# Kernel tuning notes

Hardware: AMD Instinct MI355X
Metric: run time of the kernel (lower is better)

## Reference

```python
import jax, jax.numpy as jnp
import numpy as np

N_NODES = 100000
N_EDGES = 1600000
N_GRAPHS = 1000
H = 4

def _ln(x, g, b, eps=1e-5):
    m = x.mean(-1, keepdims=True)
    v = ((x - m) ** 2).mean(-1, keepdims=True)
    return (x - m) / jnp.sqrt(v + eps) * g + b

def _gat(x, src, dst, W, att_src, att_dst, bias, C):
    # PyG GATConv (self-loops already appended to src/dst): per-edge scores,
    # segment softmax over incoming edges of each dst node, scatter-add aggregation.
    N = x.shape[0]
    h = (x @ W.T).reshape(N, H, C)                      # [N,H,C]
    a_s = (h * att_src[None]).sum(-1)                   # [N,H]
    a_d = (h * att_dst[None]).sum(-1)                   # [N,H]
    e = jax.nn.leaky_relu(a_s[src] + a_d[dst], 0.2)     # [E,H]
    m = jax.ops.segment_max(e, dst, num_segments=N)
    w = jnp.exp(e - m[dst])
    denom = jax.ops.segment_sum(w, dst, num_segments=N)
    alpha = w / denom[dst]
    out = jax.ops.segment_sum(alpha[:, :, None] * h[src], dst, num_segments=N)
    return out.reshape(N, H * C) + bias

def _mha_len1(y, in_w, in_b, out_w, out_b, d):
    # seq_len==1 (x.unsqueeze(0)): softmax over a single key is identically 1,
    # so MHA(y,y,y) == out_proj(v_proj(y)). Exactly the original math.
    v = y @ in_w[2 * d:3 * d].T + in_b[2 * d:3 * d]
    return v @ out_w.T + out_b

def _forward(x, edge_index, batch, fc_feat_w, fc_feat_b,
             gat1_w, gat1_as, gat1_ad, gat1_b,
             gat2_w, gat2_as, gat2_ad, gat2_b,
             enc_in_w, enc_in_b, enc_out_w, enc_out_b,
             enc_f1_w, enc_f1_b, enc_f2_w, enc_f2_b,
             enc_ln1_g, enc_ln1_b, enc_ln2_g, enc_ln2_b,
             dec_sa_in_w, dec_sa_in_b, dec_sa_out_w, dec_sa_out_b,
             dec_ca_in_w, dec_ca_in_b, dec_ca_out_w, dec_ca_out_b,
             dec_f1_w, dec_f1_b, dec_f2_w, dec_f2_b,
             dec_ln1_g, dec_ln1_b, dec_ln2_g, dec_ln2_b, dec_ln3_g, dec_ln3_b,
             fc_w, fc_b):
    N = x.shape[0]
    d = 16 * H  # 64
    loop = jnp.arange(N, dtype=edge_index.dtype)
    src = jnp.concatenate([edge_index[0], loop])  # add_self_loops=True (PyG default)
    dst = jnp.concatenate([edge_index[1], loop])
    h = x @ fc_feat_w.T + fc_feat_b                     # feature_fc: [N,8]
    h = jax.nn.leaky_relu(_gat(h, src, dst, gat1_w, gat1_as, gat1_ad, gat1_b, 32), 0.01)
    h = jax.nn.leaky_relu(_gat(h, src, dst, gat2_w, gat2_as, gat2_ad, gat2_b, 16), 0.01)
    y = h  # [N,64]; transformer sees (L=1, B=N, E=64)
    for i in range(2):  # encoder layers
        a = _mha_len1(y, enc_in_w[i], enc_in_b[i], enc_out_w[i], enc_out_b[i], d)
        y = _ln(y + a, enc_ln1_g[i], enc_ln1_b[i])
        f = jax.nn.relu(y @ enc_f1_w[i].T + enc_f1_b[i]) @ enc_f2_w[i].T + enc_f2_b[i]
        y = _ln(y + f, enc_ln2_g[i], enc_ln2_b[i])
    for i in range(2):  # decoder layers (memory == tgt)
        a = _mha_len1(y, dec_sa_in_w[i], dec_sa_in_b[i], dec_sa_out_w[i], dec_sa_out_b[i], d)
        y = _ln(y + a, dec_ln1_g[i], dec_ln1_b[i])
        a = _mha_len1(y, dec_ca_in_w[i], dec_ca_in_b[i], dec_ca_out_w[i], dec_ca_out_b[i], d)
        y = _ln(y + a, dec_ln2_g[i], dec_ln2_b[i])
        f = jax.nn.relu(y @ dec_f1_w[i].T + dec_f1_b[i]) @ dec_f2_w[i].T + dec_f2_b[i]
        y = _ln(y + f, dec_ln3_g[i], dec_ln3_b[i])
    sums = jax.ops.segment_sum(y, batch, num_segments=N_GRAPHS)
    cnts = jax.ops.segment_sum(jnp.ones((N,), y.dtype), batch, num_segments=N_GRAPHS)
    pooled = sums / jnp.maximum(cnts, 1.0)[:, None]     # global_mean_pool
    return pooled @ fc_w.T + fc_b

def setup_inputs() -> dict:
    key = jax.random.key(0)
    ks = iter(jax.random.split(key, 64))
    p = lambda *s: jax.random.normal(next(ks), s, dtype=jnp.float32) * 0.1
    d = 64
    inp = {
        'x': jax.random.normal(next(ks), (N_NODES, 4), dtype=jnp.float32),
        'edge_index': jax.random.randint(next(ks), (2, N_EDGES), 0, N_NODES, dtype=jnp.int32),
        'batch': jnp.sort(jax.random.randint(next(ks), (N_NODES,), 0, N_GRAPHS, dtype=jnp.int32)),
        'fc_feat_w': p(8, 4), 'fc_feat_b': p(8),
        'gat1_w': p(128, 8), 'gat1_as': p(H, 32), 'gat1_ad': p(H, 32), 'gat1_b': p(128),
        'gat2_w': p(64, 128), 'gat2_as': p(H, 16), 'gat2_ad': p(H, 16), 'gat2_b': p(64),
        'enc_in_w': p(2, 3 * d, d), 'enc_in_b': p(2, 3 * d), 'enc_out_w': p(2, d, d), 'enc_out_b': p(2, d),
        'enc_f1_w': p(2, 256, d), 'enc_f1_b': p(2, 256), 'enc_f2_w': p(2, d, 256), 'enc_f2_b': p(2, d),
        'enc_ln1_g': jnp.ones((2, d)), 'enc_ln1_b': jnp.zeros((2, d)),
        'enc_ln2_g': jnp.ones((2, d)), 'enc_ln2_b': jnp.zeros((2, d)),
        'dec_sa_in_w': p(2, 3 * d, d), 'dec_sa_in_b': p(2, 3 * d), 'dec_sa_out_w': p(2, d, d), 'dec_sa_out_b': p(2, d),
        'dec_ca_in_w': p(2, 3 * d, d), 'dec_ca_in_b': p(2, 3 * d), 'dec_ca_out_w': p(2, d, d), 'dec_ca_out_b': p(2, d),
        'dec_f1_w': p(2, 256, d), 'dec_f1_b': p(2, 256), 'dec_f2_w': p(2, d, 256), 'dec_f2_b': p(2, d),
        'dec_ln1_g': jnp.ones((2, d)), 'dec_ln1_b': jnp.zeros((2, d)),
        'dec_ln2_g': jnp.ones((2, d)), 'dec_ln2_b': jnp.zeros((2, d)),
        'dec_ln3_g': jnp.ones((2, d)), 'dec_ln3_b': jnp.zeros((2, d)),
        'fc_w': p(33, d), 'fc_b': p(33),
    }
    return inp

def reference(x, edge_index, batch, fc_feat_w, fc_feat_b,
              gat1_w, gat1_as, gat1_ad, gat1_b,
              gat2_w, gat2_as, gat2_ad, gat2_b,
              enc_in_w, enc_in_b, enc_out_w, enc_out_b,
              enc_f1_w, enc_f1_b, enc_f2_w, enc_f2_b,
              enc_ln1_g, enc_ln1_b, enc_ln2_g, enc_ln2_b,
              dec_sa_in_w, dec_sa_in_b, dec_sa_out_w, dec_sa_out_b,
              dec_ca_in_w, dec_ca_in_b, dec_ca_out_w, dec_ca_out_b,
              dec_f1_w, dec_f1_b, dec_f2_w, dec_f2_b,
              dec_ln1_g, dec_ln1_b, dec_ln2_g, dec_ln2_b, dec_ln3_g, dec_ln3_b,
              fc_w, fc_b):
    return _forward(x, edge_index, batch, fc_feat_w, fc_feat_b,
                    gat1_w, gat1_as, gat1_ad, gat1_b,
                    gat2_w, gat2_as, gat2_ad, gat2_b,
                    enc_in_w, enc_in_b, enc_out_w, enc_out_b,
                    enc_f1_w, enc_f1_b, enc_f2_w, enc_f2_b,
                    enc_ln1_g, enc_ln1_b, enc_ln2_g, enc_ln2_b,
                    dec_sa_in_w, dec_sa_in_b, dec_sa_out_w, dec_sa_out_b,
                    dec_ca_in_w, dec_ca_in_b, dec_ca_out_w, dec_ca_out_b,
                    dec_f1_w, dec_f1_b, dec_f2_w, dec_f2_b,
                    dec_ln1_g, dec_ln1_b, dec_ln2_g, dec_ln2_b, dec_ln3_g, dec_ln3_b,
                    fc_w, fc_b)
```

## Files before the change

kernel.cpp:

```cpp
#include <hip/hip_runtime.h>

#define NN 100000
#define NE 1600000
#define NG 1000
#define ETOT (NE + NN)
#define NODES_PER_GRP 12500

typedef _Float16 f16x8 __attribute__((ext_vector_type(8)));
typedef _Float16 f16x4 __attribute__((ext_vector_type(4)));
typedef _Float16 f16x2 __attribute__((ext_vector_type(2)));
typedef float f32x16 __attribute__((ext_vector_type(16)));
#define XROW 72

__global__ void k_h1(const float* __restrict__ x, const float* __restrict__ ffw,
                     const float* __restrict__ ffb, const float* __restrict__ g1w,
                     const float* __restrict__ asw, const float* __restrict__ adw,
                     _Float16* __restrict__ h1p, float* __restrict__ asp,
                     float* __restrict__ ad_) {
    int tid = blockIdx.x * 256 + threadIdx.x;
    int n = __builtin_amdgcn_readfirstlane(tid >> 6);
    int jp = threadIdx.x & 63;
    float xv[4];
#pragma unroll
    for (int k = 0; k < 4; k++) xv[k] = x[n * 4 + k];
    float h0[8];
#pragma unroll
    for (int o = 0; o < 8; o++) {
        float a = ffb[o];
#pragma unroll
        for (int k = 0; k < 4; k++) a = fmaf(xv[k], ffw[o * 4 + k], a);
        h0[o] = a;
    }
    const float* w0 = g1w + jp * 8;
    const float* w1 = g1w + (jp + 64) * 8;
    float a0 = 0.f, a1 = 0.f;
#pragma unroll
    for (int k = 0; k < 8; k++) { a0 = fmaf(h0[k], w0[k], a0); a1 = fmaf(h0[k], w1[k], a1); }
    f16x2 r; r[0] = (_Float16)a0; r[1] = (_Float16)a1;
    *(f16x2*)(h1p + ((size_t)n * 64 + jp) * 2) = r;
    float p0 = a0 * asw[jp], p1 = a1 * asw[jp + 64];
    float d0 = a0 * adw[jp], d1 = a1 * adw[jp + 64];
#pragma unroll
    for (int m = 1; m <= 16; m <<= 1) {
        p0 += __shfl_xor(p0, m, 64); p1 += __shfl_xor(p1, m, 64);
        d0 += __shfl_xor(d0, m, 64); d1 += __shfl_xor(d1, m, 64);
    }
    if ((jp & 31) == 0) {
        int half = jp >> 5;
        *(float2*)(asp + n * 4 + half * 2) = make_float2(p0, p1);
        ad_[n * 4 + half] = d0;
        ad_[n * 4 + 2 + half] = d1;
    }
}

__global__ void k_att2(const _Float16* __restrict__ h2h, const float* __restrict__ asw,
                       const float* __restrict__ adw, float* __restrict__ as_,
                       float* __restrict__ ad_) {
    int tid = blockIdx.x * 256 + threadIdx.x;
    if (tid >= NN * 4) return;
    int n = tid >> 2, h = tid & 3;
    const _Float16* hp = h2h + (size_t)n * 64 + h * 16;
    const float* ws_ = asw + h * 16;
    const float* wd_ = adw + h * 16;
    float a = 0.f, d = 0.f;
#pragma unroll
    for (int c = 0; c < 16; c++) {
        float hv = (float)hp[c];
        a = fmaf(hv, ws_[c], a); d = fmaf(hv, wd_[c], d);
    }
    as_[tid] = a; ad_[tid] = d;
}

__global__ void k_count(const int* __restrict__ ei, int* __restrict__ deg) {
    int g = blockIdx.x & 7;
    int bi = blockIdx.x >> 3;
    int nb = gridDim.x >> 3;
    int lo = g * NODES_PER_GRP, hi = lo + NODES_PER_GRP;
    int stride = nb * 256;
    for (int e = bi * 256 + threadIdx.x; e < NE; e += 4 * stride) {
        int e1 = e + stride, e2 = e + 2 * stride, e3 = e + 3 * stride;
        int d0 = __builtin_nontemporal_load(ei + NE + e);
        int d1 = (e1 < NE) ? __builtin_nontemporal_load(ei + NE + e1) : -1;
        int d2 = (e2 < NE) ? __builtin_nontemporal_load(ei + NE + e2) : -1;
        int d3 = (e3 < NE) ? __builtin_nontemporal_load(ei + NE + e3) : -1;
        if (d0 >= lo && d0 < hi) atomicAdd(&deg[d0], 1);
        if (d1 >= lo && d1 < hi) atomicAdd(&deg[d1], 1);
        if (d2 >= lo && d2 < hi) atomicAdd(&deg[d2], 1);
        if (d3 >= lo && d3 < hi) atomicAdd(&deg[d3], 1);
    }
}

__global__ void k_scan1(const int* __restrict__ deg, int* __restrict__ offs, int* __restrict__ bsum) {
    __shared__ int s[1024];
    int tid = threadIdx.x;
    int i = blockIdx.x * 1024 + tid;
    int v = (i < NN) ? deg[i] + 1 : 0;
    s[tid] = v;
    __syncthreads();
    for (int d = 1; d < 1024; d <<= 1) {
        int t = 0;
        if (tid >= d) t = s[tid - d];
        __syncthreads();
        if (tid >= d) s[tid] += t;
        __syncthreads();
    }
    if (i < NN) offs[i] = s[tid] - v;
    if (tid == 1023) bsum[blockIdx.x] = s[tid];
}

__global__ void k_scan2(int* __restrict__ bsum) {
    __shared__ int s[128];
    int tid = threadIdx.x;
    int v = (tid < 98) ? bsum[tid] : 0;
    s[tid] = v;
    __syncthreads();
    for (int d = 1; d < 128; d <<= 1) {
        int t = 0;
        if (tid >= d) t = s[tid - d];
        __syncthreads();
        if (tid >= d) s[tid] += t;
        __syncthreads();
    }
    bsum[tid] = s[tid] - v;
}

__global__ void k_scan3(int* __restrict__ offs, const int* __restrict__ bsum, int* __restrict__ cur,
                        int* __restrict__ srcs) {
    int i = blockIdx.x * 1024 + threadIdx.x;
    if (i < NN) {
        int v = offs[i] + bsum[blockIdx.x];
        offs[i] = v;
        cur[i] = v + 1;
        srcs[v] = i;
    }
    if (i == 0) offs[NN] = ETOT;
}

__global__ void k_scatter(const int* __restrict__ ei, int* __restrict__ cur,
                          int* __restrict__ srcs) {
    int g = blockIdx.x & 7;
    int bi = blockIdx.x >> 3;
    int nb = gridDim.x >> 3;
    int lo = g * NODES_PER_GRP, hi = lo + NODES_PER_GRP;
    int stride = nb * 256;
    for (int e = bi * 256 + threadIdx.x; e < NE; e += 4 * stride) {
        int e1 = e + stride, e2 = e + 2 * stride, e3 = e + 3 * stride;
        int d0 = __builtin_nontemporal_load(ei + NE + e);
        int s0 = __builtin_nontemporal_load(ei + e);
        int d1 = -1, s1 = 0, d2 = -1, s2 = 0, d3 = -1, s3 = 0;
        if (e1 < NE) { d1 = __builtin_nontemporal_load(ei + NE + e1); s1 = __builtin_nontemporal_load(ei + e1); }
        if (e2 < NE) { d2 = __builtin_nontemporal_load(ei + NE + e2); s2 = __builtin_nontemporal_load(ei + e2); }
        if (e3 < NE) { d3 = __builtin_nontemporal_load(ei + NE + e3); s3 = __builtin_nontemporal_load(ei + e3); }
        if (d0 >= lo && d0 < hi) { int p = atomicAdd(&cur[d0], 1); srcs[p] = s0; }
// ... 66 lines not shown
    int wid = __builtin_amdgcn_readfirstlane((blockIdx.x * 256 + threadIdx.x) >> 6);
    int lane = threadIdx.x & 63;
    if (wid >= NN) return;
    int off = offs[wid];
    int deg = offs[wid + 1] - off;
    int hA = lane >> 5;
    const int* sp = srcs + off;
    const uint2* wp = ew + off;
    float ws0 = 0.f, ws1 = 0.f, ac0 = 0.f, ac1 = 0.f;
    float ws0b = 0.f, ws1b = 0.f, ac0b = 0.f, ac1b = 0.f;
    int j = 0;
    for (; j + 8 <= deg; j += 8) {
        G1LD(0) G1LD(1) G1LD(2) G1LD(3) G1LD(4) G1LD(5) G1LD(6) G1LD(7)
        G1GA(0) G1GA(1) G1GA(2) G1GA(3) G1GA(4) G1GA(5) G1GA(6) G1GA(7)
        G1AC(0, ws0, ws1, ac0, ac1)     G1AC(1, ws0b, ws1b, ac0b, ac1b)
        G1AC(2, ws0, ws1, ac0, ac1)     G1AC(3, ws0b, ws1b, ac0b, ac1b)
        G1AC(4, ws0, ws1, ac0, ac1)     G1AC(5, ws0b, ws1b, ac0b, ac1b)
        G1AC(6, ws0, ws1, ac0, ac1)     G1AC(7, ws0b, ws1b, ac0b, ac1b)
    }
    if (j < deg) {
        G1LDM(0) G1LDM(1) G1LDM(2) G1LDM(3) G1LDM(4) G1LDM(5) G1LDM(6) G1LDM(7)
        G1GA(0) G1GA(1) G1GA(2) G1GA(3) G1GA(4) G1GA(5) G1GA(6) G1GA(7)
        G1AC(0, ws0, ws1, ac0, ac1)     G1AC(1, ws0b, ws1b, ac0b, ac1b)
        G1AC(2, ws0, ws1, ac0, ac1)     G1AC(3, ws0b, ws1b, ac0b, ac1b)
        G1AC(4, ws0, ws1, ac0, ac1)     G1AC(5, ws0b, ws1b, ac0b, ac1b)
        G1AC(6, ws0, ws1, ac0, ac1)     G1AC(7, ws0b, ws1b, ac0b, ac1b)
    }
    ws0 += ws0b; ws1 += ws1b; ac0 += ac0b; ac1 += ac1b;
    float v0 = ac0 / ws0 + bias[lane];      v0 = fmaxf(v0, 0.01f * v0);
    float v1 = ac1 / ws1 + bias[lane + 64]; v1 = fmaxf(v1, 0.01f * v1);
    g1h[(size_t)wid * 128 + lane] = (_Float16)v0;
    g1h[(size_t)wid * 128 + lane + 64] = (_Float16)v1;
}

#define G2LD(q)  int s##q = sp[j + q]; uint2 e##q = wp[j + q];
#define G2LDM(q) int jj##q = j + q; int jc##q = jj##q < deg ? jj##q : deg - 1; \
                 int s##q = sp[jc##q]; uint2 e##q = wp[jc##q]; \
                 if (jj##q >= deg) { e##q.x = 0u; e##q.y = 0u; }
#define G2GA(q)  float hv##q = (float)h2h[(size_t)s##q * 64 + lane];
#define G2AC(q, W, A) { \
    unsigned sel = (hd & 2) ? e##q.y : e##q.x; \
    union { unsigned u; _Float16 h[2]; } c; c.u = sel >> sh; \
    float w = (float)c.h[0]; W += w; A = fmaf(w, hv##q, A); }

__global__ void k_gat2(const int* __restrict__ offs, const int* __restrict__ srcs,
                       const uint2* __restrict__ ew, const _Float16* __restrict__ h2h,
                       const float* __restrict__ bias, _Float16* __restrict__ g2h) {
    int wid = __builtin_amdgcn_readfirstlane((blockIdx.x * 256 + threadIdx.x) >> 6);
    int lane = threadIdx.x & 63;
    if (wid >= NN) return;
    int off = offs[wid];
    int deg = offs[wid + 1] - off;
    int hd = lane >> 4;
    int sh = (hd & 1) * 16;
    const int* sp = srcs + off;
    const uint2* wp = ew + off;
    float ws = 0.f, ac = 0.f, wsb = 0.f, acb = 0.f;
    int j = 0;
    for (; j + 8 <= deg; j += 8) {
        G2LD(0) G2LD(1) G2LD(2) G2LD(3) G2LD(4) G2LD(5) G2LD(6) G2LD(7)
        G2GA(0) G2GA(1) G2GA(2) G2GA(3) G2GA(4) G2GA(5) G2GA(6) G2GA(7)
        G2AC(0, ws, ac)  G2AC(1, wsb, acb)
        G2AC(2, ws, ac)  G2AC(3, wsb, acb)
        G2AC(4, ws, ac)  G2AC(5, wsb, acb)
        G2AC(6, ws, ac)  G2AC(7, wsb, acb)
    }
    if (j < deg) {
        G2LDM(0) G2LDM(1) G2LDM(2) G2LDM(3) G2LDM(4) G2LDM(5) G2LDM(6) G2LDM(7)
        G2GA(0) G2GA(1) G2GA(2) G2GA(3) G2GA(4) G2GA(5) G2GA(6) G2GA(7)
        G2AC(0, ws, ac)  G2AC(1, wsb, acb)
        G2AC(2, ws, ac)  G2AC(3, wsb, acb)
        G2AC(4, ws, ac)  G2AC(5, wsb, acb)
        G2AC(6, ws, ac)  G2AC(7, wsb, acb)
    }
    ws += wsb; ac += acb;
    float v = ac / ws + bias[lane]; v = fmaxf(v, 0.01f * v);
    g2h[(size_t)wid * 64 + lane] = (_Float16)v;
}

#define GROW 136
#define CROW 72
__global__ __launch_bounds__(256, 2) void k_h2m(const _Float16* __restrict__ g1h,
                                                const _Float16* __restrict__ apw2,
                                                _Float16* __restrict__ h2h) {
    __shared__ _Float16 ls[4 * 32 * GROW];
    const int t = threadIdx.x;
    const int w = t >> 6, l = t & 63;
    const int col = l & 31, hf = l >> 5;
    const int wv = blockIdx.x * 4 + w;
    const int nb = wv * 32;
    if (nb >= NN) return;
    _Float16* g16 = ls + w * (32 * GROW);
    const int r = l >> 1, hb = l & 1;
    {
        int nr = nb + r; if (nr >= NN) nr = NN - 1;
        const _Float16* src = g1h + (size_t)nr * 128 + hb * 64;
        _Float16* dst = g16 + r * GROW + hb * 64;
#pragma unroll
        for (int q = 0; q < 8; q++)
            *(f16x8*)(dst + q * 8) = *(const f16x8*)(src + q * 8);
    }
    f16x8 bf[8];
#pragma unroll
    for (int ks = 0; ks < 8; ks++)
        bf[ks] = *(const f16x8*)(g16 + col * GROW + ks * 16 + hf * 8);
    f32x16 acc0, acc1;
#pragma unroll
    for (int i = 0; i < 16; i++) { acc0[i] = 0.f; acc1[i] = 0.f; }
#pragma unroll
    for (int ks = 0; ks < 8; ks++) {
        f16x8 a0 = *(const f16x8*)(apw2 + ((0 * 8 + ks) * 64 + l) * 8);
        f16x8 a1 = *(const f16x8*)(apw2 + ((1 * 8 + ks) * 64 + l) * 8);
        acc0 = __builtin_amdgcn_mfma_f32_32x32x16_f16(a0, bf[ks], acc0, 0, 0, 0);
        acc1 = __builtin_amdgcn_mfma_f32_32x32x16_f16(a1, bf[ks], acc1, 0, 0, 0);
    }
    _Float16* c16 = g16;
#pragma unroll
    for (int rg = 0; rg < 4; rg++) {
        f16x4 h0, h1;
#pragma unroll
        for (int i = 0; i < 4; i++) { h0[i] = (_Float16)acc0[rg * 4 + i]; h1[i] = (_Float16)acc1[rg * 4 + i]; }
        *(f16x4*)(c16 + col * CROW + rg * 8 + hf * 4) = h0;
        *(f16x4*)(c16 + col * CROW + 32 + rg * 8 + hf * 4) = h1;
    }
    if (nb + r < NN) {
        _Float16* dst = h2h + (size_t)(nb + r) * 64 + hb * 32;
        const _Float16* srow = c16 + r * CROW + hb * 32;
#pragma unroll
        for (int q = 0; q < 4; q++)
            *(f16x8*)(dst + q * 8) = *(const f16x8*)(srow + q * 8);
    }
}

__global__ void k_fuse(const float* __restrict__ enc_in_w, const float* __restrict__ enc_in_b,
                       const float* __restrict__ enc_out_w, const float* __restrict__ enc_out_b,
                       const float* __restrict__ sa_in_w, const float* __restrict__ sa_in_b,
                       const float* __restrict__ sa_out_w, const float* __restrict__ sa_out_b,
                       const float* __restrict__ ca_in_w, const float* __restrict__ ca_in_b,
                       const float* __restrict__ ca_out_w, const float* __restrict__ ca_out_b,
                       _Float16* __restrict__ apk, float* __restrict__ fb) {
    int tid = blockIdx.x * 256 + threadIdx.x;
    int p = tid >> 12, r = tid & 4095, j = r >> 6, k = r & 63;
    int li = p & 1;
    const float *iw, *ib, *ow, *ob;
    if (p < 2)      { iw = enc_in_w + li * 12288; ib = enc_in_b + li * 192; ow = enc_out_w + li * 4096; ob = enc_out_b + li * 64; }
    else if (p < 4) { iw = sa_in_w + li * 12288;  ib = sa_in_b + li * 192;  ow = sa_out_w + li * 4096;  ob = sa_out_b + li * 64; }
    else            { iw = ca_in_w + li * 12288;  ib = ca_in_b + li * 192;  ow = ca_out_w + li * 4096;  ob = ca_out_b + li * 64; }
    float a = 0.f;
    for (int m = 0; m < 64; m++) a = fmaf(ow[j * 64 + m], iw[(128 + m) * 64 + k], a);
    int l = ((k >> 3) & 1) * 32 + (j & 31);
    apk[p * 4096 + (((j >> 5) * 4 + (k >> 4)) * 64 + l) * 8 + (k & 7)] = (_Float16)a;
    if (k == 0) {
        float fa = ob[j];
        for (int m = 0; m < 64; m++) fa = fmaf(ow[j * 64 + m], ib[128 + m], fa);
        fb[p * 64 + j] = fa;
    }
}

#define APK_F1 24576
#define APK_F2 90112
#define APK_TOT 155648
__global__ void k_apack(const float* __restrict__ ef1, const float* __restrict__ df1,
                        const float* __restrict__ ef2, const float* __restrict__ df2,
                        const float* __restrict__ g2w, _Float16* __restrict__ apk,
                        _Float16* __restrict__ apw2) {
    int tid = blockIdx.x * 256 + threadIdx.x;
    if (tid < 65536) {
        int pl = tid >> 14, idx = tid & 16383;
        int mt = idx >> 11, ks = (idx >> 9) & 3, l = (idx >> 3) & 63, d = idx & 7;
        int m = mt * 32 + (l & 31), k = ks * 16 + (l >> 5) * 8 + d;
        const float* f1 = (pl < 2) ? ef1 + pl * 16384 : df1 + (pl - 2) * 16384;
        apk[APK_F1 + pl * 16384 + idx] = (_Float16)f1[m * 64 + k];
    } else if (tid < 131072) {
        int r = tid - 65536;
        int pl = r >> 14, idx = r & 16383;
        int mt = idx >> 13, ks = (idx >> 9) & 15, l = (idx >> 3) & 63, d = idx & 7;
        int m = mt * 32 + (l & 31), k = ks * 16 + (l >> 5) * 8 + d;
        const float* f2 = (pl < 2) ? ef2 + pl * 16384 : df2 + (pl - 2) * 16384;
        apk[APK_F2 + pl * 16384 + idx] = (_Float16)f2[m * 256 + k];
    } else {
        int r = tid - 131072;
        int mtks = r >> 9, l = (r >> 3) & 63, d = r & 7;
        int mt = mtks >> 3, ks = mtks & 7;
        int m = mt * 32 + (l & 31), k = ks * 16 + (l >> 5) * 8 + d;
        apw2[r] = (_Float16)g2w[m * 128 + k];
    }
}

struct XQ {
    const _Float16* apk; const float* fb;
    const float* ef1b; const float* ef2b; const float* df1b; const float* df2b;
    const float* el1g; const float* el1b; const float* el2g; const float* el2b;
    const float* dl1g; const float* dl1b; const float* dl2g; const float* dl2b;
    const float* dl3g; const float* dl3b;
};

__device__ __forceinline__ void xstore(_Float16* xw, const float y[4][16], int col, int hf) {
#pragma unroll
    for (int nt = 0; nt < 2; nt++)
#pragma unroll
        for (int mt = 0; mt < 2; mt++)
#pragma unroll
            for (int rg = 0; rg < 4; rg++) {
                f16x4 h4;
#pragma unroll
                for (int i = 0; i < 4; i++) h4[i] = (_Float16)y[mt * 2 + nt][rg * 4 + i];
                *(f16x4*)(xw + (nt * 32 + col) * XROW + mt * 32 + rg * 8 + hf * 4) = h4;
            }
}

__device__ __forceinline__ void loadbf(const _Float16* xw, f16x8 bf[2][4], int col, int hf) {
#pragma unroll
    for (int nt = 0; nt < 2; nt++)
#pragma unroll
        for (int ks = 0; ks < 4; ks++)
            bf[nt][ks] = *(const f16x8*)(xw + (nt * 32 + col) * XROW + ks * 16 + hf * 8);
}

__device__ __forceinline__ void lnw(float y[4][16], const float* g, const float* b, int hf) {
#pragma unroll
    for (int nt = 0; nt < 2; nt++) {
        float s = 0.f, q = 0.f;
#pragma unroll
        for (int mt = 0; mt < 2; mt++)
#pragma unroll
            for (int r = 0; r < 16; r++) { float v = y[mt * 2 + nt][r]; s += v; q = fmaf(v, v, q); }
        s += __shfl_xor(s, 32, 64);
        q += __shfl_xor(q, 32, 64);
        float m = s * 0.015625f;
        float var = fmaf(q, 0.015625f, -m * m);
        float rs = rsqrtf(var + 1e-5f);
#pragma unroll
        for (int mt = 0; mt < 2; mt++)
#pragma unroll
            for (int rg = 0; rg < 4; rg++) {
                float4 g4 = *(const float4*)(g + mt * 32 + rg * 8 + hf * 4);
                float4 b4 = *(const float4*)(b + mt * 32 + rg * 8 + hf * 4);
                float* yp = &y[mt * 2 + nt][rg * 4];
                yp[0] = fmaf((yp[0] - m) * rs, g4.x, b4.x);
                yp[1] = fmaf((yp[1] - m) * rs, g4.y, b4.y);
                yp[2] = fmaf((yp[2] - m) * rs, g4.z, b4.z);
                yp[3] = fmaf((yp[3] - m) * rs, g4.w, b4.w);
            }
    }
}

__global__ __launch_bounds__(128, 2) void k_xform(const _Float16* __restrict__ yin,
                                                  float* __restrict__ yout, XQ P) {
    __shared__ _Float16 xs[2 * 64 * XROW];
    __shared__ _Float16 wb[8192];
    const int t = threadIdx.x;
    const int w = t >> 6, l = t & 63;
    const int col = l & 31, hf = l >> 5;
    _Float16* xw = xs + w * (64 * XROW);
    const int nb = blockIdx.x * 128 + w * 64;
    const int nn0 = nb + col, nn1 = nb + 32 + col;
    const int nc0 = nn0 < NN ? nn0 : NN - 1;
    const int nc1 = nn1 < NN ? nn1 : NN - 1;

    float y[4][16];
#pragma unroll
    for (int mt = 0; mt < 2; mt++)
#pragma unroll
        for (int nt = 0; nt < 2; nt++) {
            const _Float16* src = yin + (size_t)(nt ? nc1 : nc0) * 64 + mt * 32 + hf * 4;
#pragma unroll
            for (int rg = 0; rg < 4; rg++) {
                f16x4 v = *(const f16x4*)(src + rg * 8);
#pragma unroll
                for (int i = 0; i < 4; i++) y[mt * 2 + nt][rg * 4 + i] = (float)v[i];
            }
        }
    f16x8 bf[2][4];
    xstore(xw, y, col, hf);
    loadbf(xw, bf, col, hf);

#pragma unroll 1
    for (int layer = 0; layer < 4; layer++) {
        const bool enc = layer < 2;
        const int li = enc ? layer : layer - 2;
        const int nat = enc ? 1 : 2;
#pragma unroll 1
        for (int at = 0; at < nat; at++) {
            const int p = enc ? layer : (at == 0 ? 2 + li : 4 + li);
            const _Float16* apA = P.apk + p * 4096;
            __syncthreads();
#pragma unroll
            for (int i = 0; i < 4; i++)
                *(f16x8*)(wb + (t + i * 128) * 8) = *(const f16x8*)(apA + (t + i * 128) * 8);
            __syncthreads();
            const float* fbp = P.fb + p * 64;
            f32x16 acc[4];
#pragma unroll
            for (int mt = 0; mt < 2; mt++) {
                f32x16 a;
#pragma unroll
                for (int rg = 0; rg < 4; rg++) {
                    float4 b4 = *(const float4*)(fbp + mt * 32 + rg * 8 + hf * 4);
                    a[rg * 4 + 0] = b4.x; a[rg * 4 + 1] = b4.y; a[rg * 4 + 2] = b4.z; a[rg * 4 + 3] = b4.w;
                }
                acc[mt * 2 + 0] = a; acc[mt * 2 + 1] = a;
            }
#pragma unroll
            for (int mt = 0; mt < 2; mt++)
#pragma unroll
                for (int ks = 0; ks < 4; ks++) {
                    f16x8 af = *(const f16x8*)(wb + ((mt * 4 + ks) * 64 + l) * 8);
                    acc[mt * 2 + 0] = __builtin_amdgcn_mfma_f32_32x32x16_f16(af, bf[0][ks], acc[mt * 2 + 0], 0, 0, 0);
                    acc[mt * 2 + 1] = __builtin_amdgcn_mfma_f32_32x32x16_f16(af, bf[1][ks], acc[mt * 2 + 1], 0, 0, 0);
                }
#pragma unroll
            for (int ti = 0; ti < 4; ti++)
#pragma unroll
                for (int r = 0; r < 16; r++) y[ti][r] += acc[ti][r];
            const float *g, *b;
            if (enc)          { g = P.el1g + li * 64; b = P.el1b + li * 64; }
            else if (at == 0) { g = P.dl1g + li * 64; b = P.dl1b + li * 64; }
            else              { g = P.dl2g + li * 64; b = P.dl2b + li * 64; }
            lnw(y, g, b, hf);
            xstore(xw, y, col, hf);
            loadbf(xw, bf, col, hf);
        }
        const int pl = enc ? layer : 2 + li;
        const _Float16* apF1 = P.apk + APK_F1 + pl * 16384;
        const _Float16* apF2 = P.apk + APK_F2 + pl * 16384;
        const float* f1bp = (enc ? P.ef1b : P.df1b) + li * 256;
        const float* f2bp = (enc ? P.ef2b : P.df2b) + li * 64;
        f32x16 out[4];
#pragma unroll
        for (int mt = 0; mt < 2; mt++) {
            f32x16 a;
#pragma unroll
            for (int rg = 0; rg < 4; rg++) {
                float4 b4 = *(const float4*)(f2bp + mt * 32 + rg * 8 + hf * 4);
                a[rg * 4 + 0] = b4.x; a[rg * 4 + 1] = b4.y; a[rg * 4 + 2] = b4.z; a[rg * 4 + 3] = b4.w;
            }
            out[mt * 2 + 0] = a; out[mt * 2 + 1] = a;
        }
#pragma unroll 1
        for (int c = 0; c < 4; c++) {
            __syncthreads();
#pragma unroll
            for (int i = 0; i < 4; i++)
                *(f16x8*)(wb + (t + i * 128) * 8) = *(const f16x8*)(apF1 + c * 4096 + (t + i * 128) * 8);
#pragma unroll
            for (int i = 0; i < 2; i++) {
                *(f16x8*)(wb + 4096 + (t + i * 128) * 8) = *(const f16x8*)(apF2 + c * 2048 + (t + i * 128) * 8);
                *(f16x8*)(wb + 6144 + (t + i * 128) * 8) = *(const f16x8*)(apF2 + 8192 + c * 2048 + (t + i * 128) * 8);
            }
            __syncthreads();
            f32x16 ha[4];
#pragma unroll
            for (int hmt = 0; hmt < 2; hmt++) {
                f32x16 a;
#pragma unroll
                for (int rg = 0; rg < 4; rg++) {
                    float4 b4 = *(const float4*)(f1bp + c * 64 + hmt * 32 + rg * 8 + hf * 4);
                    a[rg * 4 + 0] = b4.x; a[rg * 4 + 1] = b4.y; a[rg * 4 + 2] = b4.z; a[rg * 4 + 3] = b4.w;
                }
                ha[hmt * 2 + 0] = a; ha[hmt * 2 + 1] = a;
            }
#pragma unroll
            for (int hmt = 0; hmt < 2; hmt++)
#pragma unroll
                for (int ks = 0; ks < 4; ks++) {
                    f16x8 af = *(const f16x8*)(wb + ((hmt * 4 + ks) * 64 + l) * 8);
                    ha[hmt * 2 + 0] = __builtin_amdgcn_mfma_f32_32x32x16_f16(af, bf[0][ks], ha[hmt * 2 + 0], 0, 0, 0);
                    ha[hmt * 2 + 1] = __builtin_amdgcn_mfma_f32_32x32x16_f16(af, bf[1][ks], ha[hmt * 2 + 1], 0, 0, 0);
                }
#pragma unroll
            for (int nt = 0; nt < 2; nt++)
#pragma unroll
                for (int hmt = 0; hmt < 2; hmt++)
#pragma unroll
                    for (int rg = 0; rg < 4; rg++) {
                        f16x4 h4;
#pragma unroll
                        for (int i = 0; i < 4; i++)
                            h4[i] = (_Float16)fmaxf(ha[hmt * 2 + nt][rg * 4 + i], 0.f);
                        *(f16x4*)(xw + (nt * 32 + col) * XROW + hmt * 32 + rg * 8 + hf * 4) = h4;
                    }
#pragma unroll
            for (int ksl = 0; ksl < 4; ksl++) {
                f16x8 hbf0 = *(const f16x8*)(xw + col * XROW + ksl * 16 + hf * 8);
                f16x8 hbf1 = *(const f16x8*)(xw + (32 + col) * XROW + ksl * 16 + hf * 8);
#pragma unroll
                for (int mt = 0; mt < 2; mt++) {
                    f16x8 af = *(const f16x8*)(wb + 4096 + mt * 2048 + (ksl * 64 + l) * 8);
                    out[mt * 2 + 0] = __builtin_amdgcn_mfma_f32_32x32x16_f16(af, hbf0, out[mt * 2 + 0], 0, 0, 0);
                    out[mt * 2 + 1] = __builtin_amdgcn_mfma_f32_32x32x16_f16(af, hbf1, out[mt * 2 + 1], 0, 0, 0);
                }
            }
        }
#pragma unroll
        for (int ti = 0; ti < 4; ti++)
#pragma unroll
            for (int r = 0; r < 16; r++) y[ti][r] += out[ti][r];
        const float* g2 = (enc ? P.el2g : P.dl3g) + li * 64;
        const float* b2 = (enc ? P.el2b : P.dl3b) + li * 64;
        lnw(y, g2, b2, hf);
        if (layer < 3) {
            xstore(xw, y, col, hf);
            loadbf(xw, bf, col, hf);
        }
    }
#pragma unroll
    for (int mt = 0; mt < 2; mt++)
#pragma unroll
        for (int nt = 0; nt < 2; nt++) {
            int n = nt ? nn1 : nn0;
            if (n < NN) {
                float* dst = yout + (size_t)n * 64 + mt * 32 + hf * 4;
#pragma unroll
                for (int rg = 0; rg < 4; rg++) {
                    const float* yp = &y[mt * 2 + nt][rg * 4];
                    *(float4*)(dst + rg * 8) = make_float4(yp[0], yp[1], yp[2], yp[3]);
                }
            }
        }
}

__global__ void k_pool(const float* __restrict__ y, const int* __restrict__ batch,
                       float* __restrict__ pooled) {
    int b = blockIdx.x;
    int t = threadIdx.x;
    int ch = t & 63, r = t >> 6;
    int lo = 0, hi = NN;
    while (lo < hi) { int mid = (lo + hi) >> 1; if (batch[mid] < b) lo = mid + 1; else hi = mid; }
    int st = lo;
    hi = NN;
    while (lo < hi) { int mid = (lo + hi) >> 1; if (batch[mid] < b + 1) lo = mid + 1; else hi = mid; }
    int en = lo;
    float s = 0.f;
    for (int i = st + r; i < en; i += 4) s += y[(size_t)i * 64 + ch];
    __shared__ float red[256];
    red[t] = s;
    __syncthreads();
    if (t < 64) {
        float tot = red[t] + red[t + 64] + red[t + 128] + red[t + 192];
        int cnt = en - st; if (cnt < 1) cnt = 1;
        pooled[b * 64 + t] = tot / (float)cnt;
    }
}

__global__ void k_fc(const float* __restrict__ pooled, const float* __restrict__ fcw,
                     const float* __restrict__ fcb, float* __restrict__ out) {
    int tid = blockIdx.x * 256 + threadIdx.x;
    if (tid >= NG * 33) return;
    int g = tid / 33, o = tid - g * 33;
    const float* p = pooled + g * 64;
    const float* w = fcw + o * 64;
    float a0 = 0.f, a1 = 0.f, a2 = 0.f, a3 = 0.f;
#pragma unroll
    for (int k = 0; k < 16; k++) {
        a0 = fmaf(p[4 * k], w[4 * k], a0);
        a1 = fmaf(p[4 * k + 1], w[4 * k + 1], a1);
        a2 = fmaf(p[4 * k + 2], w[4 * k + 2], a2);
        a3 = fmaf(p[4 * k + 3], w[4 * k + 3], a3);
    }
    out[tid] = fcb[o] + (a0 + a1) + (a2 + a3);
}

extern "C" void kernel_launch(void* const* d_in, const int* in_sizes, int n_in,
                              void* d_out, int out_size, void* d_ws, size_t ws_size,
                              hipStream_t stream) {
    (void)in_sizes; (void)n_in; (void)out_size; (void)ws_size;
    char* ws = (char*)d_ws;
    size_t o = 0;
    auto A = [&](size_t b) { size_t r = o; o += (b + 255) & ~(size_t)255; return r; };
    _Float16* h1p = (_Float16*)(ws + A((size_t)NN * 128 * 2));
    _Float16* h2h = (_Float16*)(ws + A((size_t)NN * 64 * 2));
    _Float16* g1h = (_Float16*)(ws + A((size_t)NN * 128 * 2));
    _Float16* g2h = (_Float16*)(ws + A((size_t)NN * 64 * 2));
    float* f_y   = (float*)(ws + A((size_t)NN * 64 * 4));
    float* f_asp = (float*)(ws + A((size_t)NN * 4 * 4));
    float* f_ad1 = (float*)(ws + A((size_t)NN * 4 * 4));
    float* f_as2 = (float*)(ws + A((size_t)NN * 4 * 4));
    float* f_ad2 = (float*)(ws + A((size_t)NN * 4 * 4));
    int* i_off   = (int*)(ws + A((size_t)(NN + 1) * 4));
    int* i_cur   = (int*)(ws + A((size_t)NN * 4));
    int* i_deg   = (int*)(ws + A((size_t)NN * 4));
    int* i_bsum  = (int*)(ws + A((size_t)1024 * 4));
    int* i_srcs  = (int*)(ws + A((size_t)ETOT * 4));
    uint2* e_w   = (uint2*)(ws + A((size_t)ETOT * 8));
    float* f_fb  = (float*)(ws + A((size_t)6 * 64 * 4));
    _Float16* f_apk = (_Float16*)(ws + A((size_t)APK_TOT * 2));
    _Float16* apw2  = (_Float16*)(ws + A((size_t)8192 * 2));
    float* f_pool= (float*)(ws + A((size_t)NG * 64 * 4));

    const float* x   = (const float*)d_in[0];
    const int* ei    = (const int*)d_in[1];
    const int* batch = (const int*)d_in[2];
    #define F32(i) ((const float*)d_in[i])

    hipMemsetAsync(i_deg, 0, (size_t)NN * 4, stream);
    k_h1<<<NN * 64 / 256, 256, 0, stream>>>(x, F32(3), F32(4), F32(5), F32(6), F32(7),
                                            h1p, f_asp, f_ad1);
    k_count<<<8 * 256, 256, 0, stream>>>(ei, i_deg);
    k_scan1<<<98, 1024, 0, stream>>>(i_deg, i_off, i_bsum);
    k_scan2<<<1, 128, 0, stream>>>(i_bsum);
    k_scan3<<<98, 1024, 0, stream>>>(i_off, i_bsum, i_cur, i_srcs);
    k_scatter<<<8 * 256, 256, 0, stream>>>(ei, i_cur, i_srcs);
    k_ew1<<<NN * 16 / 256, 256, 0, stream>>>(i_off, i_srcs, f_asp, f_ad1, e_w);
    k_gat1<<<NN * 64 / 256, 256, 0, stream>>>(i_off, i_srcs, e_w, h1p, F32(8), g1h);
    k_apack<<<544, 256, 0, stream>>>(F32(17), F32(33), F32(19), F32(35), F32(9), f_apk, apw2);
    k_h2m<<<(NN / 32 + 3) / 4, 256, 0, stream>>>(g1h, apw2, h2h);
    k_att2<<<(NN * 4 + 255) / 256, 256, 0, stream>>>(h2h, F32(10), F32(11), f_as2, f_ad2);
    k_ew2<<<NN * 16 / 256, 256, 0, stream>>>(i_off, i_srcs, f_as2, f_ad2, e_w);
    k_gat2<<<NN * 64 / 256, 256, 0, stream>>>(i_off, i_srcs, e_w, h2h, F32(12), g2h);
    k_fuse<<<24576 / 256, 256, 0, stream>>>(F32(13), F32(14), F32(15), F32(16),
                                            F32(25), F32(26), F32(27), F32(28),
                                            F32(29), F32(30), F32(31), F32(32),
                                            f_apk, f_fb);
    XQ Q;
    Q.apk = f_apk; Q.fb = f_fb;
    Q.ef1b = F32(18); Q.ef2b = F32(20);
    Q.df1b = F32(34); Q.df2b = F32(36);
    Q.el1g = F32(21); Q.el1b = F32(22); Q.el2g = F32(23); Q.el2b = F32(24);
    Q.dl1g = F32(37); Q.dl1b = F32(38); Q.dl2g = F32(39); Q.dl2b = F32(40);
    Q.dl3g = F32(41); Q.dl3b = F32(42);
    k_xform<<<(NN + 127) / 128, 128, 0, stream>>>(g2h, f_y, Q);
    k_pool<<<NG, 256, 0, stream>>>(f_y, batch, f_pool);
    k_fc<<<(NG * 33 + 255) / 256, 256, 0, stream>>>(f_pool, F32(43), F32(44), (float*)d_out);
    #undef F32
}
```

Baseline: 591.4 us.

## Fuse small kernels, compute attention logits in MFMA epilogue, prefetch xform weights

Folds the degree memset into k_h1, computes the layer-2 attention source/destination scores inside k_h2m from the MFMA accumulators, and merges k_fuse with k_apack and k_pool with k_fc. This removes several launches and a full re-read of h2h. k_xform now uses 256-thread blocks and prefetches the next weight tile into registers while the current one is in use, which raises register and LDS pressure.

New measurement: 575.7 us. 2.7% less time.

```diff
diff --git a/kernel.cpp b/kernel.cpp
--- a/kernel.cpp
+++ b/kernel.cpp
@@ -16,8 +16,9 @@
                      const float* __restrict__ ffb, const float* __restrict__ g1w,
                      const float* __restrict__ asw, const float* __restrict__ adw,
                      _Float16* __restrict__ h1p, float* __restrict__ asp,
-                     float* __restrict__ ad_) {
+                     float* __restrict__ ad_, int* __restrict__ deg) {
     int tid = blockIdx.x * 256 + threadIdx.x;
+    if (tid < NN) deg[tid] = 0;
     int n = __builtin_amdgcn_readfirstlane(tid >> 6);
     int jp = threadIdx.x & 63;
     float xv[4];
@@ -51,24 +52,6 @@
         ad_[n * 4 + half] = d0;
         ad_[n * 4 + 2 + half] = d1;
     }
-}
-
-__global__ void k_att2(const _Float16* __restrict__ h2h, const float* __restrict__ asw,
-                       const float* __restrict__ adw, float* __restrict__ as_,
-                       float* __restrict__ ad_) {
-    int tid = blockIdx.x * 256 + threadIdx.x;
-    if (tid >= NN * 4) return;
-    int n = tid >> 2, h = tid & 3;
-    const _Float16* hp = h2h + (size_t)n * 64 + h * 16;
-    const float* ws_ = asw + h * 16;
-    const float* wd_ = adw + h * 16;
-    float a = 0.f, d = 0.f;
-#pragma unroll
-    for (int c = 0; c < 16; c++) {
-        float hv = (float)hp[c];
-        a = fmaf(hv, ws_[c], a); d = fmaf(hv, wd_[c], d);
-    }
-    as_[tid] = a; ad_[tid] = d;
 }
 
 __global__ void k_count(const int* __restrict__ ei, int* __restrict__ deg) {
@@ -301,7 +284,11 @@
 #define CROW 72
 __global__ __launch_bounds__(256, 2) void k_h2m(const _Float16* __restrict__ g1h,
                                                 const _Float16* __restrict__ apw2,
-                                                _Float16* __restrict__ h2h) {
+                                                const float* __restrict__ asw,
+                                                const float* __restrict__ adw,
+                                                _Float16* __restrict__ h2h,
+                                                float* __restrict__ as_,
+                                                float* __restrict__ ad_) {
     __shared__ _Float16 ls[4 * 32 * GROW];
     const int t = threadIdx.x;
     const int w = t >> 6, l = t & 63;
@@ -333,6 +320,33 @@
         acc0 = __builtin_amdgcn_mfma_f32_32x32x16_f16(a0, bf[ks], acc0, 0, 0, 0);
         acc1 = __builtin_amdgcn_mfma_f32_32x32x16_f16(a1, bf[ks], acc1, 0, 0, 0);
     }
+    {
+        float pa0 = 0.f, pa1 = 0.f, pa2 = 0.f, pa3 = 0.f;
+        float pd0 = 0.f, pd1 = 0.f, pd2 = 0.f, pd3 = 0.f;
+#pragma unroll
+        for (int rg = 0; rg < 4; rg++)
+#pragma unroll
+            for (int i = 0; i < 4; i++) {
+                int rr = rg * 4 + i;
+                int f = i + rg * 8 + hf * 4;
+                float h0v = (float)(_Float16)acc0[rr];
+                float h1v = (float)(_Float16)acc1[rr];
+                float s0 = asw[f], d0v = adw[f];
+                float s1 = asw[32 + f], d1v = adw[32 + f];
+                if (rg < 2) { pa0 = fmaf(h0v, s0, pa0); pd0 = fmaf(h0v, d0v, pd0);
+                              pa2 = fmaf(h1v, s1, pa2); pd2 = fmaf(h1v, d1v, pd2); }
+                else        { pa1 = fmaf(h0v, s0, pa1); pd1 = fmaf(h0v, d0v, pd1);
+                              pa3 = fmaf(h1v, s1, pa3); pd3 = fmaf(h1v, d1v, pd3); }
+            }
+        pa0 += __shfl_xor(pa0, 32, 64); pa1 += __shfl_xor(pa1, 32, 64);
+        pa2 += __shfl_xor(pa2, 32, 64); pa3 += __shfl_xor(pa3, 32, 64);
+        pd0 += __shfl_xor(pd0, 32, 64); pd1 += __shfl_xor(pd1, 32, 64);
+        pd2 += __shfl_xor(pd2, 32, 64); pd3 += __shfl_xor(pd3, 32, 64);
+        if (hf == 0 && nb + col < NN) {
+            *(float4*)(as_ + (size_t)(nb + col) * 4) = make_float4(pa0, pa1, pa2, pa3);
+            *(float4*)(ad_ + (size_t)(nb + col) * 4) = make_float4(pd0, pd1, pd2, pd3);
+        }
+    }
     _Float16* c16 = g16;
 #pragma unroll
     for (int rg = 0; rg < 4; rg++) {
@@ -351,58 +365,60 @@
     }
 }
 
-__global__ void k_fuse(const float* __restrict__ enc_in_w, const float* __restrict__ enc_in_b,
+#define APK_F1 24576
+#define APK_F2 90112
+#define APK_TOT 155648
+__global__ void k_prep(const float* __restrict__ enc_in_w, const float* __restrict__ enc_in_b,
                        const float* __restrict__ enc_out_w, const float* __restrict__ enc_out_b,
                        const float* __restrict__ sa_in_w, const float* __restrict__ sa_in_b,
                        const float* __restrict__ sa_out_w, const float* __restrict__ sa_out_b,
                        const float* __restrict__ ca_in_w, const float* __restrict__ ca_in_b,
                        const float* __restrict__ ca_out_w, const float* __restrict__ ca_out_b,
-                       _Float16* __restrict__ apk, float* __restrict__ fb) {
-    int tid = blockIdx.x * 256 + threadIdx.x;
-    int p = tid >> 12, r = tid & 4095, j = r >> 6, k = r & 63;
-    int li = p & 1;
-    const float *iw, *ib, *ow, *ob;
-    if (p < 2)      { iw = enc_in_w + li * 12288; ib = enc_in_b + li * 192; ow = enc_out_w + li * 4096; ob = enc_out_b + li * 64; }
-    else if (p < 4) { iw = sa_in_w + li * 12288;  ib = sa_in_b + li * 192;  ow = sa_out_w + li * 4096;  ob = sa_out_b + li * 64; }
-    else            { iw = ca_in_w + li * 12288;  ib = ca_in_b + li * 192;  ow = ca_out_w + li * 4096;  ob = ca_out_b + li * 64; }
-    float a = 0.f;
-    for (int m = 0; m < 64; m++) a = fmaf(ow[j * 64 + m], iw[(128 + m) * 64 + k], a);
-    int l = ((k >> 3) & 1) * 32 + (j & 31);
-    apk[p * 4096 + (((j >> 5) * 4 + (k >> 4)) * 64 + l) * 8 + (k & 7)] = (_Float16)a;
-    if (k == 0) {
-        float fa = ob[j];
-        for (int m = 0; m < 64; m++) fa = fmaf(ow[j * 64 + m], ib[128 + m], fa);
-        fb[p * 64 + j] = fa;
-    }
-}
-
-#define APK_F1 24576
-#define APK_F2 90112
-#define APK_TOT 155648
-__global__ void k_apack(const float* __restrict__ ef1, const float* __restrict__ df1,
-                        const float* __restrict__ ef2, const float* __restrict__ df2,
-                        const float* __restrict__ g2w, _Float16* __restrict__ apk,
-                        _Float16* __restrict__ apw2) {
-    int tid = blockIdx.x * 256 + threadIdx.x;
-    if (tid < 65536) {
-        int pl = tid >> 14, idx = tid & 16383;
-        int mt = idx >> 11, ks = (idx >> 9) & 3, l = (idx >> 3) & 63, d = idx & 7;
-        int m = mt * 32 + (l & 31), k = ks * 16 + (l >> 5) * 8 + d;
-        const float* f1 = (pl < 2) ? ef1 + pl * 16384 : df1 + (pl - 2) * 16384;
-        apk[APK_F1 + pl * 16384 + idx] = (_Float16)f1[m * 64 + k];
-    } else if (tid < 131072) {
-        int r = tid - 65536;
-        int pl = r >> 14, idx = r & 16383;
-        int mt = idx >> 13, ks = (idx >> 9) & 15, l = (idx >> 3) & 63, d = idx & 7;
-        int m = mt * 32 + (l & 31), k = ks * 16 + (l >> 5) * 8 + d;
-        const float* f2 = (pl < 2) ? ef2 + pl * 16384 : df2 + (pl - 2) * 16384;
-        apk[APK_F2 + pl * 16384 + idx] = (_Float16)f2[m * 256 + k];
+                       const float* __restrict__ ef1, const float* __restrict__ df1,
+                       const float* __restrict__ ef2, const float* __restrict__ df2,
+                       const float* __restrict__ g2w,
+                       _Float16* __restrict__ apk, float* __restrict__ fb,
+                       _Float16* __restrict__ apw2) {
+    int gt = blockIdx.x * 256 + threadIdx.x;
+    if (gt < 24576) {
+        int tid = gt;
+        int p = tid >> 12, rr = tid & 4095, j = rr >> 6, k = rr & 63;
+        int li = p & 1;
+        const float *iw, *ib, *ow, *ob;
+        if (p < 2)      { iw = enc_in_w + li * 12288; ib = enc_in_b + li * 192; ow = enc_out_w + li * 4096; ob = enc_out_b + li * 64; }
+        else if (p < 4) { iw = sa_in_w + li * 12288;  ib = sa_in_b + li * 192;  ow = sa_out_w + li * 4096;  ob = sa_out_b + li * 64; }
+        else            { iw = ca_in_w + li * 12288;  ib = ca_in_b + li * 192;  ow = ca_out_w + li * 4096;  ob = ca_out_b + li * 64; }
+        float a = 0.f;
+        for (int m = 0; m < 64; m++) a = fmaf(ow[j * 64 + m], iw[(128 + m) * 64 + k], a);
+        int l = ((k >> 3) & 1) * 32 + (j & 31);
+        apk[p * 4096 + (((j >> 5) * 4 + (k >> 4)) * 64 + l) * 8 + (k & 7)] = (_Float16)a;
+        if (k == 0) {
+            float fa = ob[j];
+            for (int m = 0; m < 64; m++) fa = fmaf(ow[j * 64 + m], ib[128 + m], fa);
+            fb[p * 64 + j] = fa;
+        }
     } else {
-        int r = tid - 131072;
-        int mtks = r >> 9, l = (r >> 3) & 63, d = r & 7;
-        int mt = mtks >> 3, ks = mtks & 7;
-        int m = mt * 32 + (l & 31), k = ks * 16 + (l >> 5) * 8 + d;
-        apw2[r] = (_Float16)g2w[m * 128 + k];
+        int tid = gt - 24576;
+        if (tid < 65536) {
+            int pl = tid >> 14, idx = tid & 16383;
+            int mt = idx >> 11, ks = (idx >> 9) & 3, l = (idx >> 3) & 63, d = idx & 7;
+            int m = mt * 32 + (l & 31), k = ks * 16 + (l >> 5) * 8 + d;
+            const float* f1 = (pl < 2) ? ef1 + pl * 16384 : df1 + (pl - 2) * 16384;
+            apk[APK_F1 + pl * 16384 + idx] = (_Float16)f1[m * 64 + k];
+        } else if (tid < 131072) {
+            int rr = tid - 65536;
+            int pl = rr >> 14, idx = rr & 16383;
+            int mt = idx >> 13, ks = (idx >> 9) & 15, l = (idx >> 3) & 63, d = idx & 7;
+            int m = mt * 32 + (l & 31), k = ks * 16 + (l >> 5) * 8 + d;
+            const float* f2 = (pl < 2) ? ef2 + pl * 16384 : df2 + (pl - 2) * 16384;
+            apk[APK_F2 + pl * 16384 + idx] = (_Float16)f2[m * 256 + k];
+        } else {
+            int rr = tid - 131072;
+            int mtks = rr >> 9, l = (rr >> 3) & 63, d = rr & 7;
+            int mt = mtks >> 3, ks = mtks & 7;
+            int m = mt * 32 + (l & 31), k = ks * 16 + (l >> 5) * 8 + d;
+            apw2[rr] = (_Float16)g2w[m * 128 + k];
+        }
     }
 }
 
@@ -464,15 +480,15 @@
     }
 }
 
-__global__ __launch_bounds__(128, 2) void k_xform(const _Float16* __restrict__ yin,
+__global__ __launch_bounds__(256, 2) void k_xform(const _Float16* __restrict__ yin,
                                                   float* __restrict__ yout, XQ P) {
-    __shared__ _Float16 xs[2 * 64 * XROW];
+    __shared__ _Float16 xs[4 * 64 * XROW];
     __shared__ _Float16 wb[8192];
     const int t = threadIdx.x;
     const int w = t >> 6, l = t & 63;
     const int col = l & 31, hf = l >> 5;
     _Float16* xw = xs + w * (64 * XROW);
-    const int nb = blockIdx.x * 128 + w * 64;
+    const int nb = blockIdx.x * 256 + w * 64;
     const int nn0 = nb + col, nn1 = nb + 32 + col;
     const int nc0 = nn0 < NN ? nn0 : NN - 1;
     const int nc1 = nn1 < NN ? nn1 : NN - 1;
@@ -493,21 +509,39 @@
     f16x8 bf[2][4];
     xstore(xw, y, col, hf);
     loadbf(xw, bf, col, hf);
+
+    f16x8 r0, r1, r2, r3;
+    {
+        const _Float16* apA = P.apk;
+        r0 = *(const f16x8*)(apA + t * 8);
+        r1 = *(const f16x8*)(apA + (t + 256) * 8);
+    }
 
 #pragma unroll 1
     for (int layer = 0; layer < 4; layer++) {
         const bool enc = layer < 2;
         const int li = enc ? layer : layer - 2;
         const int nat = enc ? 1 : 2;
+        const int pl = enc ? layer : 2 + li;
+        const _Float16* apF1 = P.apk + APK_F1 + pl * 16384;
+        const _Float16* apF2 = P.apk + APK_F2 + pl * 16384;
 #pragma unroll 1
         for (int at = 0; at < nat; at++) {
             const int p = enc ? layer : (at == 0 ? 2 + li : 4 + li);
-            const _Float16* apA = P.apk + p * 4096;
             __syncthreads();
-#pragma unroll
-            for (int i = 0; i < 4; i++)
-                *(f16x8*)(wb + (t + i * 128) * 8) = *(const f16x8*)(apA + (t + i * 128) * 8);
+            *(f16x8*)(wb + t * 8) = r0;
+            *(f16x8*)(wb + (t + 256) * 8) = r1;
             __syncthreads();
+            if (at < nat - 1) {
+                const _Float16* apN = P.apk + (4 + li) * 4096;
+                r0 = *(const f16x8*)(apN + t * 8);
+                r1 = *(const f16x8*)(apN + (t + 256) * 8);
+            } else {
+                r0 = *(const f16x8*)(apF1 + t * 8);
+                r1 = *(const f16x8*)(apF1 + (t + 256) * 8);
+                r2 = *(const f16x8*)(apF2 + t * 8);
+                r3 = *(const f16x8*)(apF2 + 8192 + t * 8);
+            }
             const float* fbp = P.fb + p * 64;
             f32x16 acc[4];
 #pragma unroll
@@ -540,9 +574,6 @@
             xstore(xw, y, col, hf);
             loadbf(xw, bf, col, hf);
         }
-        const int pl = enc ? layer : 2 + li;
-        const _Float16* apF1 = P.apk + APK_F1 + pl * 16384;
-        const _Float16* apF2 = P.apk + APK_F2 + pl * 16384;
         const float* f1bp = (enc ? P.ef1b : P.df1b) + li * 256;
         const float* f2bp = (enc ? P.ef2b : P.df2b) + li * 64;
         f32x16 out[4];
@@ -559,15 +590,21 @@
 #pragma unroll 1
         for (int c = 0; c < 4; c++) {
             __syncthreads();
-#pragma unroll
-            for (int i = 0; i < 4; i++)
-                *(f16x8*)(wb + (t + i * 128) * 8) = *(const f16x8*)(apF1 + c * 4096 + (t + i * 128) * 8);
-#pragma unroll
-            for (int i = 0; i < 2; i++) {
-                *(f16x8*)(wb + 4096 + (t + i * 128) * 8) = *(const f16x8*)(apF2 + c * 2048 + (t + i * 128) * 8);
-                *(f16x8*)(wb + 6144 + (t + i * 128) * 8) = *(const f16x8*)(apF2 + 8192 + c * 2048 + (t + i * 128) * 8);
-            }
+            *(f16x8*)(wb + t * 8) = r0;
+            *(f16x8*)(wb + (t + 256) * 8) = r1;
+            *(f16x8*)(wb + 4096 + t * 8) = r2;
+            *(f16x8*)(wb + 6144 + t * 8) = r3;
             __syncthreads();
+            if (c < 3) {
+                r0 = *(const f16x8*)(apF1 + (c + 1) * 4096 + t * 8);
+                r1 = *(const f16x8*)(apF1 + (c + 1) * 4096 + (t + 256) * 8);
+                r2 = *(const f16x8*)(apF2 + (c + 1) * 2048 + t * 8);
+                r3 = *(const f16x8*)(apF2 + 8192 + (c + 1) * 2048 + t * 8);
+            } else if (layer < 3) {
+                const _Float16* apN = P.apk + (layer + 1) * 4096;
+                r0 = *(const f16x8*)(apN + t * 8);
+                r1 = *(const f16x8*)(apN + (t + 256) * 8);
+            }
             f32x16 ha[4];
 #pragma unroll
             for (int hmt = 0; hmt < 2; hmt++) {
@@ -640,7 +677,8 @@
 }
 
 __global__ void k_pool(const float* __restrict__ y, const int* __restrict__ batch,
-                       float* __restrict__ pooled) {
+                       const float* __restrict__ fcw, const float* __restrict__ fcb,
+                       float* __restrict__ out) {
     int b = blockIdx.x;
     int t = threadIdx.x;
     int ch = t & 63, r = t >> 6;
@@ -653,31 +691,27 @@
     float s = 0.f;
     for (int i = st + r; i < en; i += 4) s += y[(size_t)i * 64 + ch];
     __shared__ float red[256];
+    __shared__ float pl[64];
     red[t] = s;
     __syncthreads();
     if (t < 64) {
         float tot = red[t] + red[t + 64] + red[t + 128] + red[t + 192];
         int cnt = en - st; if (cnt < 1) cnt = 1;
-        pooled[b * 64 + t] = tot / (float)cnt;
-    }
-}
-
-__global__ void k_fc(const float* __restrict__ pooled, const float* __restrict__ fcw,
-                     const float* __restrict__ fcb, float* __restrict__ out) {
-    int tid = blockIdx.x * 256 + threadIdx.x;
-    if (tid >= NG * 33) return;
-    int g = tid / 33, o = tid - g * 33;
-    const float* p = pooled + g * 64;
-    const float* w = fcw + o * 64;
-    float a0 = 0.f, a1 = 0.f, a2 = 0.f, a3 = 0.f;
-#pragma unroll
-    for (int k = 0; k < 16; k++) {
-        a0 = fmaf(p[4 * k], w[4 * k], a0);
-        a1 = fmaf(p[4 * k + 1], w[4 * k + 1], a1);
-        a2 = fmaf(p[4 * k + 2], w[4 * k + 2], a2);
-        a3 = fmaf(p[4 * k + 3], w[4 * k + 3], a3);
-    }
-    out[tid] = fcb[o] + (a0 + a1) + (a2 + a3);
+        pl[t] = tot / (float)cnt;
+    }
+    __syncthreads();
+    if (t < 33) {
+        const float* wv = fcw + t * 64;
+        float a0 = 0.f, a1 = 0.f, a2 = 0.f, a3 = 0.f;
+#pragma unroll
+        for (int k = 0; k < 16; k++) {
+            a0 = fmaf(pl[4 * k], wv[4 * k], a0);
+            a1 = fmaf(pl[4 * k + 1], wv[4 * k + 1], a1);
+            a2 = fmaf(pl[4 * k + 2], wv[4 * k + 2], a2);
+            a3 = fmaf(pl[4 * k + 3], wv[4 * k + 3], a3);
+        }
+        out[b * 33 + t] = fcb[t] + (a0 + a1) + (a2 + a3);
+    }
 }
 
 extern "C" void kernel_launch(void* const* d_in, const int* in_sizes, int n_in,
@@ -705,16 +739,14 @@
     float* f_fb  = (float*)(ws + A((size_t)6 * 64 * 4));
     _Float16* f_apk = (_Float16*)(ws + A((size_t)APK_TOT * 2));
     _Float16* apw2  = (_Float16*)(ws + A((size_t)8192 * 2));
-    float* f_pool= (float*)(ws + A((size_t)NG * 64 * 4));
 
     const float* x   = (const float*)d_in[0];
     const int* ei    = (const int*)d_in[1];
     const int* batch = (const int*)d_in[2];
     #define F32(i) ((const float*)d_in[i])
 
-    hipMemsetAsync(i_deg, 0, (size_t)NN * 4, stream);
     k_h1<<<NN * 64 / 256, 256, 0, stream>>>(x, F32(3), F32(4), F32(5), F32(6), F32(7),
-                                            h1p, f_asp, f_ad1);
+                                            h1p, f_asp, f_ad1, i_deg);
     k_count<<<8 * 256, 256, 0, stream>>>(ei, i_deg);
     k_scan1<<<98, 1024, 0, stream>>>(i_deg, i_off, i_bsum);
     k_scan2<<<1, 128, 0, stream>>>(i_bsum);
@@ -722,15 +754,14 @@
     k_scatter<<<8 * 256, 256, 0, stream>>>(ei, i_cur, i_srcs);
     k_ew1<<<NN * 16 / 256, 256, 0, stream>>>(i_off, i_srcs, f_asp, f_ad1, e_w);
     k_gat1<<<NN * 64 / 256, 256, 0, stream>>>(i_off, i_srcs, e_w, h1p, F32(8), g1h);
-    k_apack<<<544, 256, 0, stream>>>(F32(17), F32(33), F32(19), F32(35), F32(9), f_apk, apw2);
-    k_h2m<<<(NN / 32 + 3) / 4, 256, 0, stream>>>(g1h, apw2, h2h);
-    k_att2<<<(NN * 4 + 255) / 256, 256, 0, stream>>>(h2h, F32(10), F32(11), f_as2, f_ad2);
+    k_prep<<<640, 256, 0, stream>>>(F32(13), F32(14), F32(15), F32(16),
+                                    F32(25), F32(26), F32(27), F32(28),
+                                    F32(29), F32(30), F32(31), F32(32),
+                                    F32(17), F32(33), F32(19), F32(35), F32(9),
+                                    f_apk, f_fb, apw2);
+    k_h2m<<<(NN / 32 + 3) / 4, 256, 0, stream>>>(g1h, apw2, F32(10), F32(11), h2h, f_as2, f_ad2);
     k_ew2<<<NN * 16 / 256, 256, 0, stream>>>(i_off, i_srcs, f_as2, f_ad2, e_w);
     k_gat2<<<NN * 64 / 256, 256, 0, stream>>>(i_off, i_srcs, e_w, h2h, F32(12), g2h);
-    k_fuse<<<24576 / 256, 256, 0, stream>>>(F32(13), F32(14), F32(15), F32(16),
-                                            F32(25), F32(26), F32(27), F32(28),
-                                            F32(29), F32(30), F32(31), F32(32),
-                                            f_apk, f_fb);
     XQ Q;
     Q.apk = f_apk; Q.fb = f_fb;
     Q.ef1b = F32(18); Q.ef2b = F32(20);
@@ -738,8 +769,7 @@
     Q.el1g = F32(21); Q.el1b = F32(22); Q.el2g = F32(23); Q.el2b = F32(24);
     Q.dl1g = F32(37); Q.dl1b = F32(38); Q.dl2g = F32(39); Q.dl2b = F32(40);
     Q.dl3g = F32(41); Q.dl3b = F32(42);
-    k_xform<<<(NN + 127) / 128, 128, 0, stream>>>(g2h, f_y, Q);
-    k_pool<<<NG, 256, 0, stream>>>(f_y, batch, f_pool);
-    k_fc<<<(NG * 33 + 255) / 256, 256, 0, stream>>>(f_pool, F32(43), F32(44), (float*)d_out);
+    k_xform<<<(NN + 255) / 256, 256, 0, stream>>>(g2h, f_y, Q);
+    k_pool<<<NG, 256, 0, stream>>>(f_y, batch, F32(43), F32(44), (float*)d_out);
     #undef F32
 }
```
